# Optimization experiments

Measured on AMD Instinct MI355X. Metric: run time of the kernel, lower is better.

The kernel has to match this reference:

```python
import jax, jax.numpy as jnp
import numpy as np

# constants from __init__ defaults
K_WINNERS = 5
GAIN_UP = 1.8
MIN_GAIN = 0.5
MAX_GAIN = 2.5
THETA = 1.0

B, T = 512, 8192


def setup_inputs() -> dict:
    key = jax.random.key(0)
    k1, k2, k3 = jax.random.split(key, 3)
    amp = jax.random.uniform(k1, (B, T), jnp.float32)
    pitch = jax.random.uniform(k2, (B, T), jnp.float32)
    boundary = jax.random.uniform(k3, (B, T), jnp.float32)
    decay = jnp.array([0.7, 0.7, 0.7], jnp.float32)    # buffer 'decay'
    weights = jnp.array([1.0, 1.0, 1.0], jnp.float32)  # buffer 'weights'
    return {"amp": amp, "pitch": pitch, "boundary": boundary,
            "decay": decay, "weights": weights}


def reference(amp, pitch, boundary, decay, weights):
    # Stack the 3 channels so one scan handles all LIF neurons: xs [3, B, T]
    xs = jnp.stack([amp, pitch, boundary], axis=0)
    d = decay[:, None]  # [3, 1] broadcast over batch

    def step(v, x_t):          # v, x_t: [3, B]
        v = d * v + x_t
        s = (v >= THETA).astype(v.dtype)
        return v - s * THETA, s

    v0 = jnp.zeros((3, B), xs.dtype)
    _, spikes = jax.lax.scan(step, v0, jnp.moveaxis(xs, 2, 0))  # spikes [T, 3, B]

    # salience = w_amp*s_amp + w_pitch*s_pitch + w_bound*s_bound -> [B, T]
    sal = jnp.einsum('c,tcb->bt', weights, spikes)
    # smoothing == 0 -> conv branch skipped (matches default init)
    sal = sal / (jnp.max(sal, axis=1, keepdims=True) + 1e-6)

    topk_vals, topk_idx = jax.lax.top_k(sal, K_WINNERS)  # [B, K]
    avg_winner = topk_vals.mean(axis=1)                  # [B]
    mu_scalar = MIN_GAIN + (MAX_GAIN - MIN_GAIN) * jnp.tanh(GAIN_UP * avg_winner)
    return mu_scalar, sal, topk_idx
```

## Files before the change

kernel.cpp:

```cpp
#include <hip/hip_runtime.h>
#include <cstdint>
#include <cstddef>

#define BB 512
#define TT 8192
#define TW 256
#define KWIN 5
#define WUP 128
#define PADROW 8256

static __device__ __forceinline__ float fract_f(float x) {
#if __has_builtin(__builtin_amdgcn_fractf)
    return __builtin_amdgcn_fractf(x);
#else
    return x - floorf(x);
#endif
}

__global__ __launch_bounds__(64, 1)
void lif_scan_kernel(const float* __restrict__ amp,
                     const float* __restrict__ pitch,
                     const float* __restrict__ boundary,
                     const float* __restrict__ decay,
                     float* __restrict__ out)
{
    const int blk = blockIdx.x;
    const int c   = blk >> 9;
    const int b   = blk & 511;
    const int l   = threadIdx.x;
    const float* __restrict__ src =
        (c == 0 ? amp : (c == 1 ? pitch : boundary)) + (size_t)b * TT;
    const float dv = decay[c];

    __shared__ float X[PADROW];

    const float4* src4 = reinterpret_cast<const float4*>(src);
#pragma unroll
    for (int g = 0; g < 2; ++g) {
        float4 st[16];
#pragma unroll
        for (int i = 0; i < 16; ++i)
            st[i] = src4[64 * (16 * g + i) + l];
#pragma unroll
        for (int i = 0; i < 16; ++i) {
            const int j0 = 4 * (64 * (16 * g + i) + l);
            const int a0 = j0 + (j0 >> 7);
            X[a0 + 0] = st[i].x;
            X[a0 + 1] = st[i].y;
            X[a0 + 2] = st[i].z;
            X[a0 + 3] = st[i].w;
        }
    }
    asm volatile("s_waitcnt lgkmcnt(0)" ::: "memory");

    float v = 0.0f;
    {
        const bool zero_in = (l == 0);
        const float* wup = &X[zero_in ? 0 : 129 * (l - 1)];
#pragma unroll
        for (int t = 0; t < WUP; ++t) {
            float x = wup[t];
            if (zero_in) x = 0.0f;
            float t2 = __fadd_rn(__fmul_rn(dv, v), x);
            v = fract_f(t2);
        }
    }
    uint32_t w[4];
    {
        const float* kp = &X[129 * l];
#pragma unroll
        for (int q = 0; q < 4; ++q) {
            float bs = 0.0f;
#pragma unroll
            for (int t = 32 * q; t < 32 * q + 16; ++t) {
                float t2 = __fadd_rn(__fmul_rn(dv, v), kp[t]);
                float nv = fract_f(t2);
                bs = __builtin_fmaf(2.0f, bs, t2 - nv);
                v = nv;
            }
            uint32_t hi = (uint32_t)bs;
            bs = 0.0f;
#pragma unroll
            for (int t = 32 * q + 16; t < 32 * q + 32; ++t) {
                float t2 = __fadd_rn(__fmul_rn(dv, v), kp[t]);
                float nv = fract_f(t2);
                bs = __builtin_fmaf(2.0f, bs, t2 - nv);
                v = nv;
            }
            w[q] = (hi << 16) | (uint32_t)bs;
        }
    }
    uint32_t* wout = reinterpret_cast<uint32_t*>(out + 512 + (size_t)b * TT)
                   + c * TW;
    *reinterpret_cast<uint4*>(wout + 4 * l) = make_uint4(w[0], w[1], w[2], w[3]);
}

__global__ __launch_bounds__(256, 2)
void salience_topk_kernel(const float* __restrict__ weights,
                          float* __restrict__ out)
{
    const int b = blockIdx.x;
    const int tid = threadIdx.x;

    __shared__ uint32_t words[3 * TW];
    __shared__ uint32_t spres[4];
    __shared__ float ntab[8];
    __shared__ uint32_t htab[8];
    __shared__ unsigned long long red[4];
    __shared__ unsigned long long wins;

    float* sal_out = out + 512 + (size_t)b * TT;
    const uint32_t* wsrc = reinterpret_cast<const uint32_t*>(sal_out);

    words[tid]       = wsrc[tid];
    words[tid + 256] = wsrc[tid + 256];
    words[tid + 512] = wsrc[tid + 512];

    const float w0 = weights[0], w1 = weights[1], w2 = weights[2];
    __syncthreads();

    uint32_t pres = 0;
#pragma unroll
    for (int j = 0; j < 8; ++j) {
        const int t0 = 4 * tid + 1024 * j;
        const int wi = t0 >> 5;
        const uint32_t wa = words[wi], wp = words[TW + wi], wq = words[2 * TW + wi];
#pragma unroll
        for (int k = 0; k < 4; ++k) {
            const int sh = 31 - ((t0 & 31) + k);
            const uint32_t idx = ((wa >> sh) & 1u)
                               | (((wp >> sh) & 1u) << 1)
                               | (((wq >> sh) & 1u) << 2);
            pres |= (1u << idx);
        }
    }
#pragma unroll
    for (int off = 32; off; off >>= 1)
        pres |= __shfl_down(pres, off);
    if ((tid & 63) == 0) spres[tid >> 6] = pres;
    __syncthreads();

    if (tid < 8) {
        const uint32_t p = spres[0] | spres[1] | spres[2] | spres[3];
        float s0 = (float)(tid & 1), s1 = (float)((tid >> 1) & 1), s2 = (float)(tid >> 2);
        float tv = __fadd_rn(__fadd_rn(__fmul_rn(w0, s0), __fmul_rn(w1, s1)),
                             __fmul_rn(w2, s2));
        float m = ((p >> tid) & 1u) ? tv : -INFINITY;
        m = fmaxf(m, __shfl_xor(m, 1));
        m = fmaxf(m, __shfl_xor(m, 2));
        m = fmaxf(m, __shfl_xor(m, 4));
        const float denom = __fadd_rn(m, 1e-6f);
        float nv = tv / denom;
        ntab[tid] = nv;
        uint32_t ub = __float_as_uint(nv);
        htab[tid] = (ub & 0x80000000u) ? ~ub : (ub | 0x80000000u);
    }
    __syncthreads();

    unsigned long long t5[5] = {0ull, 0ull, 0ull, 0ull, 0ull};
#pragma unroll
    for (int j = 0; j < 8; ++j) {
        const int t0 = 4 * tid + 1024 * j;
        const int wi = t0 >> 5;
        const uint32_t wa = words[wi], wp = words[TW + wi], wq = words[2 * TW + wi];
        float4 q;
        float* qp = &q.x;
#pragma unroll
        for (int k = 0; k < 4; ++k) {
            const int sh = 31 - ((t0 & 31) + k);
            const uint32_t idx = ((wa >> sh) & 1u)
                               | (((wp >> sh) & 1u) << 1)
                               | (((wq >> sh) & 1u) << 2);
            qp[k] = ntab[idx];
            unsigned long long key = ((unsigned long long)htab[idx] << 32)
                                   | (unsigned long long)(uint32_t)(TT - 1 - (t0 + k));
            if (key > t5[4]) {
#pragma unroll
                for (int i = 0; i < 5; ++i) {
                    bool g = key > t5[i];
                    unsigned long long o = t5[i];
                    t5[i] = g ? key : o;
                    key   = g ? o : key;
                }
            }
        }
        *reinterpret_cast<float4*>(sal_out + t0) = q;
    }

    float vsum = 0.0f;
    for (int r = 0; r < KWIN; ++r) {
        unsigned long long cand = t5[0];
#pragma unroll
        for (int off = 32; off; off >>= 1) {
            unsigned long long o = __shfl_down(cand, off);
            if (o > cand) cand = o;
        }
        __syncthreads();
        if ((tid & 63) == 0) red[tid >> 6] = cand;
        __syncthreads();
        if (tid == 0) {
            unsigned long long m = red[0];
            if (red[1] > m) m = red[1];
            if (red[2] > m) m = red[2];
            if (red[3] > m) m = red[3];
            wins = m;
        }
        __syncthreads();
        const unsigned long long w = wins;
        if (t5[0] == w) {
            t5[0] = t5[1]; t5[1] = t5[2]; t5[2] = t5[3]; t5[3] = t5[4]; t5[4] = 0ull;
        }
        if (tid == 0) {
            uint32_t hi = (uint32_t)(w >> 32);
            uint32_t fb = (hi & 0x80000000u) ? (hi & 0x7FFFFFFFu) : ~hi;
            vsum += __uint_as_float(fb);
            out[512 + (size_t)BB * TT + (size_t)b * KWIN + r] =
                (float)(int)(TT - 1 - (uint32_t)(w & 0xFFFFFFFFull));
        }
    }

    if (tid == 0) {
        out[b] = 0.5f + 2.0f * tanhf(1.8f * (vsum / 5.0f));
    }
}

extern "C" void kernel_launch(void* const* d_in, const int* in_sizes, int n_in,
                              void* d_out, int out_size, void* d_ws, size_t ws_size,
                              hipStream_t stream) {
    const float* amp      = (const float*)d_in[0];
    const float* pitch    = (const float*)d_in[1];
    const float* boundary = (const float*)d_in[2];
    const float* decay    = (const float*)d_in[3];
    const float* weights  = (const float*)d_in[4];
    float* out = (float*)d_out;

    lif_scan_kernel<<<3 * BB, 64, 0, stream>>>(amp, pitch, boundary, decay, out);
    salience_topk_kernel<<<BB, 256, 0, stream>>>(weights, out);
}
```

Before: 111.1 us.

## Keep LIF chunk in registers and fetch warm-up inputs via lane shuffles

Each lane now loads its own contiguous 128-element chunk directly into 32 float4 registers instead of staging the whole row through padded shared memory. The warm-up pass reads the previous lane's inputs with __shfl_up rather than LDS reads. Launch bounds move to 2 waves per SIMD. The intent is to drop the LDS staging and its bank-conflict padding, at the cost of high register pressure, uncoalesced per-lane strided global loads, and a cross-lane shuffle on every warm-up step.

```diff
diff --git a/kernel.cpp b/kernel.cpp
--- a/kernel.cpp
+++ b/kernel.cpp
@@ -6,8 +6,6 @@
 #define TT 8192
 #define TW 256
 #define KWIN 5
-#define WUP 128
-#define PADROW 8256
 
 static __device__ __forceinline__ float fract_f(float x) {
 #if __has_builtin(__builtin_amdgcn_fractf)
@@ -17,7 +15,7 @@
 #endif
 }
 
-__global__ __launch_bounds__(64, 1)
+__global__ __launch_bounds__(64, 2)
 void lif_scan_kernel(const float* __restrict__ amp,
                      const float* __restrict__ pitch,
                      const float* __restrict__ boundary,
@@ -32,64 +30,53 @@
         (c == 0 ? amp : (c == 1 ? pitch : boundary)) + (size_t)b * TT;
     const float dv = decay[c];
 
-    __shared__ float X[PADROW];
-
-    const float4* src4 = reinterpret_cast<const float4*>(src);
-#pragma unroll
-    for (int g = 0; g < 2; ++g) {
-        float4 st[16];
-#pragma unroll
-        for (int i = 0; i < 16; ++i)
-            st[i] = src4[64 * (16 * g + i) + l];
-#pragma unroll
-        for (int i = 0; i < 16; ++i) {
-            const int j0 = 4 * (64 * (16 * g + i) + l);
-            const int a0 = j0 + (j0 >> 7);
-            X[a0 + 0] = st[i].x;
-            X[a0 + 1] = st[i].y;
-            X[a0 + 2] = st[i].z;
-            X[a0 + 3] = st[i].w;
-        }
-    }
-    asm volatile("s_waitcnt lgkmcnt(0)" ::: "memory");
+    const float4* __restrict__ w4 = reinterpret_cast<const float4*>(src) + 32 * l;
+    float4 W[32];
+#pragma unroll
+    for (int i = 0; i < 32; ++i) W[i] = w4[i];
 
     float v = 0.0f;
-    {
-        const bool zero_in = (l == 0);
-        const float* wup = &X[zero_in ? 0 : 129 * (l - 1)];
-#pragma unroll
-        for (int t = 0; t < WUP; ++t) {
-            float x = wup[t];
-            if (zero_in) x = 0.0f;
-            float t2 = __fadd_rn(__fmul_rn(dv, v), x);
-            v = fract_f(t2);
-        }
-    }
+
+    const bool z = (l == 0);
+#define WSTEP(xx)                                               \
+    {                                                           \
+        float xw = __shfl_up((xx), 1);                          \
+        if (z) xw = 0.0f;                                       \
+        float t2 = __fadd_rn(__fmul_rn(dv, v), xw);             \
+        v = fract_f(t2);                                        \
+    }
+#pragma unroll
+    for (int i = 0; i < 32; ++i) {
+        WSTEP(W[i].x) WSTEP(W[i].y) WSTEP(W[i].z) WSTEP(W[i].w)
+    }
+#undef WSTEP
+
     uint32_t w[4];
-    {
-        const float* kp = &X[129 * l];
-#pragma unroll
-        for (int q = 0; q < 4; ++q) {
-            float bs = 0.0f;
-#pragma unroll
-            for (int t = 32 * q; t < 32 * q + 16; ++t) {
-                float t2 = __fadd_rn(__fmul_rn(dv, v), kp[t]);
-                float nv = fract_f(t2);
-                bs = __builtin_fmaf(2.0f, bs, t2 - nv);
-                v = nv;
-            }
-            uint32_t hi = (uint32_t)bs;
-            bs = 0.0f;
-#pragma unroll
-            for (int t = 32 * q + 16; t < 32 * q + 32; ++t) {
-                float t2 = __fadd_rn(__fmul_rn(dv, v), kp[t]);
-                float nv = fract_f(t2);
-                bs = __builtin_fmaf(2.0f, bs, t2 - nv);
-                v = nv;
-            }
-            w[q] = (hi << 16) | (uint32_t)bs;
-        }
-    }
+    float bs;
+#define KSTEP(xx)                                               \
+    {                                                           \
+        float t2 = __fadd_rn(__fmul_rn(dv, v), (xx));           \
+        float nv = fract_f(t2);                                 \
+        bs = __builtin_fmaf(2.0f, bs, t2 - nv);                 \
+        v = nv;                                                 \
+    }
+#pragma unroll
+    for (int q = 0; q < 4; ++q) {
+        bs = 0.0f;
+#pragma unroll
+        for (int i = 8 * q; i < 8 * q + 4; ++i) {
+            KSTEP(W[i].x) KSTEP(W[i].y) KSTEP(W[i].z) KSTEP(W[i].w)
+        }
+        const uint32_t hi = (uint32_t)bs;
+        bs = 0.0f;
+#pragma unroll
+        for (int i = 8 * q + 4; i < 8 * q + 8; ++i) {
+            KSTEP(W[i].x) KSTEP(W[i].y) KSTEP(W[i].z) KSTEP(W[i].w)
+        }
+        w[q] = (hi << 16) | (uint32_t)bs;
+    }
+#undef KSTEP
+
     uint32_t* wout = reinterpret_cast<uint32_t*>(out + 512 + (size_t)b * TT)
                    + c * TW;
     *reinterpret_cast<uint4*>(wout + 4 * l) = make_uint4(w[0], w[1], w[2], w[3]);
```

Measured after the change: 114.6 us. +3.2%, slower.
